# Performance work log

Hardware: AMD Instinct MI355X
Metric: run time of the kernel (lower is better)

Reference implementation:

```python
import jax, jax.numpy as jnp
import numpy as np

B, S, D, H = 512, 64, 1024, 16  # seq_len=64 fixed by Reshape([-1,8,8,d_model])
DH = D // H


def setup_inputs() -> dict:
    key = jax.random.key(0)
    ks = jax.random.split(key, 5)
    w_scale = 0.02  # keep pre-softmax logits / activations in a sane range
    return {
        "x": jax.random.normal(ks[0], (B, S, D), jnp.float32),
        "wq_w": jax.random.normal(ks[1], (D, D), jnp.float32) * w_scale,
        "wq_b": jnp.zeros((D,), jnp.float32),
        "wk_w": jax.random.normal(ks[2], (D, D), jnp.float32) * w_scale,
        "wk_b": jnp.zeros((D,), jnp.float32),
        "wv_w": jax.random.normal(ks[3], (D, D), jnp.float32) * w_scale,
        "wv_b": jnp.zeros((D,), jnp.float32),
        "wo_w": jax.random.normal(ks[4], (D, D), jnp.float32) * w_scale,
        "wo_b": jnp.zeros((D,), jnp.float32),
    }


def _split_heads(t):
    # [B, S, D] -> [B, H, S, DH]
    b, s, _ = t.shape
    return t.reshape(b, s, H, DH).transpose(0, 2, 1, 3)


def reference(x, wq_w, wq_b, wk_w, wk_b, wv_w, wv_b, wo_w, wo_b):
    b, s, d = x.shape
    q = _split_heads(x @ wq_w + wq_b)
    k = _split_heads(x @ wk_w + wk_b)
    v = _split_heads(x @ wv_w + wv_b)
    # NOTE: original scales by sqrt(d_model), not sqrt(depth)
    scores = jnp.einsum("bhqd,bhkd->bhqk", q, k) / jnp.sqrt(jnp.float32(d))
    # original 'padding mask': (scores == 0) * 1e-9 added to scores
    scores = scores + (scores == 0).astype(scores.dtype) * 1e-9
    attn = jax.nn.softmax(scores, axis=-1)
    ctx = jnp.einsum("bhqk,bhkd->bhqd", attn, v)  # [B, H, S, DH]
    ctx = ctx.transpose(0, 2, 1, 3).reshape(b, s, d)  # [B, S, D]
    # keras Dense(..., activation='gelu') uses exact (erf) gelu by default
    out = jax.nn.gelu(ctx @ wo_w + wo_b, approximate=False)
    # Reshape([-1, 8, 8, D]) then squeeze -> [B, 8, 8, D]
    return out.reshape(b, 8, 8, d)
```

## Files before the change

### kernel.cpp

```cpp
#include <hip/hip_runtime.h>
#include <cstdint>
#include <math.h>

typedef float f32x4 __attribute__((ext_vector_type(4)));
typedef __bf16 bf16x8 __attribute__((ext_vector_type(8)));
typedef unsigned short u16x8 __attribute__((ext_vector_type(8)));
typedef unsigned short u16x4 __attribute__((ext_vector_type(4)));

typedef __attribute__((address_space(1))) const void* gas_cvptr;
typedef __attribute__((address_space(3))) void* las_vptr;

#define WAITV8 asm volatile("s_waitcnt vmcnt(8)" ::: "memory")
#define WAITV4 asm volatile("s_waitcnt vmcnt(4)" ::: "memory")
#define WAITV0 asm volatile("s_waitcnt vmcnt(0)" ::: "memory")
#define WAITL0 asm volatile("s_waitcnt lgkmcnt(0)" ::: "memory")
#define WAITL4 asm volatile("s_waitcnt lgkmcnt(4)" ::: "memory")
#define SB()   __builtin_amdgcn_sched_barrier(0)
#define BAR()  __builtin_amdgcn_s_barrier()

__device__ __forceinline__ unsigned short f32_to_bf16(float f) {
  uint32_t u = __builtin_bit_cast(uint32_t, f);
  u += 0x7FFFu + ((u >> 16) & 1u);
  return (unsigned short)(u >> 16);
}

__device__ __forceinline__ bf16x8 ld_bf16x8(const unsigned short* p) {
  return __builtin_bit_cast(bf16x8, *(const u16x8*)p);
}

__global__ void cvt_x(const float* __restrict__ x, unsigned short* __restrict__ xb, int n4) {
  int stride = gridDim.x * blockDim.x;
  for (int i = blockIdx.x * blockDim.x + threadIdx.x; i < n4; i += stride) {
    float4 v = ((const float4*)x)[i];
    u16x4 o = { f32_to_bf16(v.x), f32_to_bf16(v.y), f32_to_bf16(v.z), f32_to_bf16(v.w) };
    ((u16x4*)xb)[i] = o;
  }
}

__global__ void cvt_w(const float* __restrict__ wq, const float* __restrict__ wk,
                      const float* __restrict__ wv, const float* __restrict__ wo,
                      unsigned short* __restrict__ wqkvT, unsigned short* __restrict__ woT) {
  const int z = blockIdx.z;
  const float* __restrict__ w = (z == 0) ? wq : (z == 1) ? wk : (z == 2) ? wv : wo;
  unsigned short* __restrict__ out = (z < 3) ? (wqkvT + (size_t)z * 1024 * 1024) : woT;
  __shared__ float tile[64][65];
  const int r0 = blockIdx.y * 64;
  const int c0 = blockIdx.x * 64;
  const int t = threadIdx.x;
#pragma unroll
  for (int i = 0; i < 4; i++) {
    int row = (t >> 4) + i * 16;
    int col = (t & 15) * 4;
    float4 v = *(const float4*)&w[(size_t)(r0 + row) * 1024 + c0 + col];
    tile[row][col] = v.x; tile[row][col + 1] = v.y;
    tile[row][col + 2] = v.z; tile[row][col + 3] = v.w;
  }
  __syncthreads();
#pragma unroll
  for (int i = 0; i < 2; i++) {
    int nr = (t >> 3) + i * 32;
    int kc = (t & 7) * 8;
    u16x8 o;
#pragma unroll
    for (int j = 0; j < 8; j++) o[j] = f32_to_bf16(tile[kc + j][nr]);
    *(u16x8*)&out[(size_t)(c0 + nr) * 1024 + r0 + kc] = o;
  }
}

template <int EPI>
__global__ __launch_bounds__(512, 2) void gemm256(
    const unsigned short* __restrict__ A, const unsigned short* __restrict__ Bt,
    const float* __restrict__ b0, const float* __restrict__ b1, const float* __restrict__ b2,
    unsigned short* __restrict__ Qb, unsigned short* __restrict__ Kb, unsigned short* __restrict__ Vb,
    float* __restrict__ Out, int Ncols, int K) {
  __shared__ __align__(16) unsigned short As[4][256][32];
  __shared__ __align__(16) unsigned short Bs[4][256][32];
  const int NT = K >> 5;
  const int nb = Ncols >> 8;
  const int nwg = gridDim.x;
  const int cpx = nwg >> 3;
  const int bid = blockIdx.x;
  const int wg = (bid & 7) * cpx + (bid >> 3);
  const int tm = wg / nb, tn = wg % nb;
  const int rowBase = tm << 8, colBase = tn << 8;
  const int t = threadIdx.x;
  const int lane = t & 63;
  const int w = t >> 6;
  const int li = lane & 15, lg = lane >> 4;
  const int wm = w >> 2, wn = w & 3;
  const int aRow0 = wm * 128;
  const int bRow0 = wn * 64;
  const int koff = ((lg ^ ((li >> 1) & 3)) << 3);

  const int c0 = t, c1 = t + 512;
  const int r0s = c0 >> 2, r1s = c1 >> 2;
  const int l0s = (c0 & 3) ^ ((r0s >> 1) & 3);
  const int l1s = (c1 & 3) ^ ((r1s >> 1) & 3);
  const unsigned short* gA0 = A + (size_t)(rowBase + r0s) * K + l0s * 8;
  const unsigned short* gA1 = A + (size_t)(rowBase + r1s) * K + l1s * 8;
  const unsigned short* gB0 = Bt + (size_t)(colBase + r0s) * K + l0s * 8;
  const unsigned short* gB1 = Bt + (size_t)(colBase + r1s) * K + l1s * 8;

#define STAGE_A(tile_) do { int b_ = (tile_) & 3; int kt_ = (tile_) << 5;                     \
    __builtin_amdgcn_global_load_lds((gas_cvptr)(gA0 + kt_),                                  \
        (las_vptr)(&As[b_][0][0] + c0 * 8), 16, 0, 0);                                        \
    __builtin_amdgcn_global_load_lds((gas_cvptr)(gA1 + kt_),                                  \
        (las_vptr)(&As[b_][0][0] + c1 * 8), 16, 0, 0); } while (0)
#define STAGE_B(tile_) do { int b_ = (tile_) & 3; int kt_ = (tile_) << 5;                     \
    __builtin_amdgcn_global_load_lds((gas_cvptr)(gB0 + kt_),                                  \
        (las_vptr)(&Bs[b_][0][0] + c0 * 8), 16, 0, 0);                                        \
    __builtin_amdgcn_global_load_lds((gas_cvptr)(gB1 + kt_),                                  \
        (las_vptr)(&Bs[b_][0][0] + c1 * 8), 16, 0, 0); } while (0)

  STAGE_A(0); STAGE_B(0);
  STAGE_A(1); STAGE_B(1);
  STAGE_A(2); STAGE_B(2);
  WAITV8;
  BAR();

  f32x4 acc[8][4] = {};

  for (int tt = 0; tt < NT; ++tt) {
    const unsigned short* ab = &As[tt & 3][0][0];
    const unsigned short* bb = &Bs[tt & 3][0][0];
    bf16x8 afA[4], bfrA[4], afB[4];
#pragma unroll
    for (int m = 0; m < 4; m++) afA[m] = ld_bf16x8(ab + (aRow0 + m * 16 + li) * 32 + koff);
#pragma unroll
    for (int n = 0; n < 4; n++) bfrA[n] = ld_bf16x8(bb + (bRow0 + n * 16 + li) * 32 + koff);
#pragma unroll
    for (int m = 0; m < 4; m++)
      afB[m] = ld_bf16x8(ab + (aRow0 + 64 + m * 16 + li) * 32 + koff);
    if (tt + 3 < NT) { STAGE_A(tt + 3); STAGE_B(tt + 3); }
    WAITL4;
    SB();
    __builtin_amdgcn_s_setprio(1);
#pragma unroll
    for (int m = 0; m < 4; m++)
#pragma unroll
      for (int n = 0; n < 4; n++)
        acc[m][n] = __builtin_amdgcn_mfma_f32_16x16x32_bf16(afA[m], bfrA[n], acc[m][n], 0, 0, 0);
    SB();
    WAITL0;
    SB();
#pragma unroll
    for (int m = 0; m < 4; m++)
#pragma unroll
      for (int n = 0; n < 4; n++)
        acc[4 + m][n] = __builtin_amdgcn_mfma_f32_16x16x32_bf16(afB[m], bfrA[n], acc[4 + m][n], 0, 0, 0);
    __builtin_amdgcn_s_setprio(0);
    if (tt <= NT - 4)      WAITV8;
    else if (tt == NT - 3) WAITV4;
    else                   WAITV0;
    BAR();
  }
#undef STAGE_A
#undef STAGE_B

  if (EPI == 0) {
    const int part = colBase >> 10;
    const float* __restrict__ bias = (part == 0) ? b0 : (part == 1) ? b1 : b2;
    unsigned short* __restrict__ dst = (part == 0) ? Qb : (part == 1) ? Kb : Vb;
#pragma unroll
    for (int mi = 0; mi < 8; mi++) {
      const int rowb = rowBase + aRow0 + mi * 16 + lg * 4;
#pragma unroll
      for (int r = 0; r < 4; r++) {
        const int row = rowb + r;
        const int b = row >> 6, s = row & 63;
#pragma unroll
        for (int n = 0; n < 4; n++) {
          const int col = colBase + bRow0 + n * 16 + li;
          const int within = col & 1023;
          const int h = within >> 6, dh = within & 63;
          float v = acc[mi][n][r] + bias[within];
          dst[(size_t)((b * 16 + h) * 64 + s) * 64 + dh] = f32_to_bf16(v);
        }
      }
    }
  } else {
#pragma unroll
    for (int mi = 0; mi < 8; mi++) {
      const int rowb = rowBase + aRow0 + mi * 16 + lg * 4;
#pragma unroll
      for (int r = 0; r < 4; r++) {
#pragma unroll
        for (int n = 0; n < 4; n++) {
          const int col = colBase + bRow0 + n * 16 + li;
          float v = acc[mi][n][r] + b0[col];
          v = 0.5f * v * (1.0f + erff(v * 0.70710678118654752f));
          Out[(size_t)(rowb + r) * 1024 + col] = v;
        }
      }
    }
  }
}

__global__ __launch_bounds__(256) void attn(
    const unsigned short* __restrict__ Qb, const unsigned short* __restrict__ Kb,
    const unsigned short* __restrict__ Vb, unsigned short* __restrict__ ctx) {
  __shared__ __align__(16) unsigned short Qs[64][72];
  __shared__ __align__(16) unsigned short Ks[64][72];
  __shared__ __align__(16) unsigned short Vt[64][72];
  __shared__ __align__(16) unsigned short Ps[64][72];
  const int bh = blockIdx.x;
  const int b = bh >> 4, h = bh & 15;
  const int t = threadIdx.x, lane = t & 63, w = t >> 6;
  const int li = lane & 15, lg = lane >> 4;
  const unsigned short* __restrict__ Qg = Qb + (size_t)bh * 4096;
  const unsigned short* __restrict__ Kg = Kb + (size_t)bh * 4096;
  const unsigned short* __restrict__ Vg = Vb + (size_t)bh * 4096;

#pragma unroll
  for (int i = 0; i < 2; i++) {
    const int c = t + i * 256;
    const int row = c >> 3, col8 = (c & 7) * 8;
    *(u16x8*)&Qs[row][col8] = *(const u16x8*)&Qg[row * 64 + col8];
    *(u16x8*)&Ks[row][col8] = *(const u16x8*)&Kg[row * 64 + col8];
    u16x8 v = *(const u16x8*)&Vg[row * 64 + col8];
#pragma unroll
    for (int j = 0; j < 8; j++) Vt[col8 + j][row] = v[j];
  }
  __syncthreads();

  f32x4 sc[4] = {};
#pragma unroll
  for (int ks = 0; ks < 2; ks++) {
    bf16x8 qa = ld_bf16x8(&Qs[w * 16 + li][ks * 32 + lg * 8]);
#pragma unroll
    for (int n = 0; n < 4; n++) {
      bf16x8 kf = ld_bf16x8(&Ks[n * 16 + li][ks * 32 + lg * 8]);
      sc[n] = __builtin_amdgcn_mfma_f32_16x16x32_bf16(qa, kf, sc[n], 0, 0, 0);
    }
  }

#pragma unroll
  for (int r = 0; r < 4; r++) {
    float v0 = sc[0][r] * 0.03125f, v1 = sc[1][r] * 0.03125f;
    float v2 = sc[2][r] * 0.03125f, v3 = sc[3][r] * 0.03125f;
    float mx = fmaxf(fmaxf(v0, v1), fmaxf(v2, v3));
#pragma unroll
    for (int off = 1; off < 16; off <<= 1) mx = fmaxf(mx, __shfl_xor(mx, off, 64));
    float e0 = __expf(v0 - mx), e1 = __expf(v1 - mx);
    float e2 = __expf(v2 - mx), e3 = __expf(v3 - mx);
    float sum = e0 + e1 + e2 + e3;
#pragma unroll
    for (int off = 1; off < 16; off <<= 1) sum += __shfl_xor(sum, off, 64);
    float is = 1.0f / sum;
    const int q = w * 16 + lg * 4 + r;
    Ps[q][0 * 16 + li] = f32_to_bf16(e0 * is);
    Ps[q][1 * 16 + li] = f32_to_bf16(e1 * is);
    Ps[q][2 * 16 + li] = f32_to_bf16(e2 * is);
    Ps[q][3 * 16 + li] = f32_to_bf16(e3 * is);
  }
  __syncthreads();

  f32x4 oc[4] = {};
#pragma unroll
  for (int ks = 0; ks < 2; ks++) {
    bf16x8 pa = ld_bf16x8(&Ps[w * 16 + li][ks * 32 + lg * 8]);
#pragma unroll
    for (int n = 0; n < 4; n++) {
      bf16x8 vf = ld_bf16x8(&Vt[n * 16 + li][ks * 32 + lg * 8]);
      oc[n] = __builtin_amdgcn_mfma_f32_16x16x32_bf16(pa, vf, oc[n], 0, 0, 0);
    }
  }
#pragma unroll
  for (int n = 0; n < 4; n++)
#pragma unroll
    for (int r = 0; r < 4; r++)
      ctx[(size_t)(b * 64 + w * 16 + lg * 4 + r) * 1024 + h * 64 + n * 16 + li] =
          f32_to_bf16(oc[n][r]);
}

extern "C" void kernel_launch(void* const* d_in, const int* in_sizes, int n_in,
                              void* d_out, int out_size, void* d_ws, size_t ws_size,
                              hipStream_t stream) {
  const float* x  = (const float*)d_in[0];
  const float* wq = (const float*)d_in[1];
  const float* bq = (const float*)d_in[2];
  const float* wk = (const float*)d_in[3];
  const float* bk = (const float*)d_in[4];
  const float* wv = (const float*)d_in[5];
  const float* bv = (const float*)d_in[6];
  const float* wo = (const float*)d_in[7];
  const float* bo = (const float*)d_in[8];
  float* out = (float*)d_out;

  const int D = 1024;
  const int M = in_sizes[0] / D;

  char* ws = (char*)d_ws;
  unsigned short* xb    = (unsigned short*)ws;
  unsigned short* wqkvT = (unsigned short*)(ws + (size_t)M * 1024 * 2);
  unsigned short* woT   = wqkvT + (size_t)3 * 1024 * 1024;
  unsigned short* Qb    = woT + (size_t)1024 * 1024;
  unsigned short* Kb    = Qb + (size_t)M * 1024;
  unsigned short* Vb    = Kb + (size_t)M * 1024;
  unsigned short* ctx   = xb;

  cvt_x<<<2048, 256, 0, stream>>>(x, xb, M * D / 4);
  cvt_w<<<dim3(16, 16, 4), 256, 0, stream>>>(wq, wk, wv, wo, wqkvT, woT);
  gemm256<0><<<(M / 256) * (3072 / 256), 512, 0, stream>>>(
      xb, wqkvT, bq, bk, bv, Qb, Kb, Vb, nullptr, 3072, 1024);
  attn<<<(M / 64) * 16, 256, 0, stream>>>(Qb, Kb, Vb, ctx);
  gemm256<1><<<(M / 256) * (1024 / 256), 512, 0, stream>>>(
      ctx, woT, bo, nullptr, nullptr, nullptr, nullptr, nullptr, out, 1024, 1024);
}
```

Before: 410.4 us.

## Deepen GEMM prefetch to four tiles and double-buffer LDS fragments in registers

The main GEMM loop now keeps four K-tiles of global-to-LDS loads in flight instead of three, using all four LDS buffers. It also adds two register fragment sets that alternate between tiles. The fragments for the next tile are read from LDS after the barrier, while the second half of the current tile's MFMAs run. The aim is to hide LDS read latency and global load latency behind matrix work. The cost is roughly double the fragment register usage under a 512-thread, 2-blocks-per-CU launch bound, and more complex wait-count logic.

```diff
diff --git a/kernel.cpp b/kernel.cpp
--- a/kernel.cpp
+++ b/kernel.cpp
@@ -10,11 +10,11 @@
 typedef __attribute__((address_space(1))) const void* gas_cvptr;
 typedef __attribute__((address_space(3))) void* las_vptr;
 
+#define WAITV12 asm volatile("s_waitcnt vmcnt(12)" ::: "memory")
 #define WAITV8 asm volatile("s_waitcnt vmcnt(8)" ::: "memory")
 #define WAITV4 asm volatile("s_waitcnt vmcnt(4)" ::: "memory")
 #define WAITV0 asm volatile("s_waitcnt vmcnt(0)" ::: "memory")
 #define WAITL0 asm volatile("s_waitcnt lgkmcnt(0)" ::: "memory")
-#define WAITL4 asm volatile("s_waitcnt lgkmcnt(4)" ::: "memory")
 #define SB()   __builtin_amdgcn_sched_barrier(0)
 #define BAR()  __builtin_amdgcn_s_barrier()
 
@@ -65,6 +65,20 @@
     for (int j = 0; j < 8; j++) o[j] = f32_to_bf16(tile[kc + j][nr]);
     *(u16x8*)&out[(size_t)(c0 + nr) * 1024 + r0 + kc] = o;
   }
+}
+
+struct Frags { bf16x8 afA[4], bfr[4], afB[4]; };
+
+__device__ __forceinline__ void read_frags(Frags& f, const unsigned short* ab,
+                                           const unsigned short* bb, int aRow0,
+                                           int bRow0, int li, int koff) {
+#pragma unroll
+  for (int m = 0; m < 4; m++) f.afA[m] = ld_bf16x8(ab + (aRow0 + m * 16 + li) * 32 + koff);
+#pragma unroll
+  for (int n = 0; n < 4; n++) f.bfr[n] = ld_bf16x8(bb + (bRow0 + n * 16 + li) * 32 + koff);
+#pragma unroll
+  for (int m = 0; m < 4; m++)
+    f.afB[m] = ld_bf16x8(ab + (aRow0 + 64 + m * 16 + li) * 32 + koff);
 }
 
 template <int EPI>
@@ -101,61 +115,58 @@
   const unsigned short* gB0 = Bt + (size_t)(colBase + r0s) * K + l0s * 8;
   const unsigned short* gB1 = Bt + (size_t)(colBase + r1s) * K + l1s * 8;
 
-#define STAGE_A(tile_) do { int b_ = (tile_) & 3; int kt_ = (tile_) << 5;                     \
+#define STAGE_AB(tile_) do { int b_ = (tile_) & 3; int kt_ = (tile_) << 5;                    \
     __builtin_amdgcn_global_load_lds((gas_cvptr)(gA0 + kt_),                                  \
         (las_vptr)(&As[b_][0][0] + c0 * 8), 16, 0, 0);                                        \
     __builtin_amdgcn_global_load_lds((gas_cvptr)(gA1 + kt_),                                  \
-        (las_vptr)(&As[b_][0][0] + c1 * 8), 16, 0, 0); } while (0)
-#define STAGE_B(tile_) do { int b_ = (tile_) & 3; int kt_ = (tile_) << 5;                     \
+        (las_vptr)(&As[b_][0][0] + c1 * 8), 16, 0, 0);                                        \
     __builtin_amdgcn_global_load_lds((gas_cvptr)(gB0 + kt_),                                  \
         (las_vptr)(&Bs[b_][0][0] + c0 * 8), 16, 0, 0);                                        \
     __builtin_amdgcn_global_load_lds((gas_cvptr)(gB1 + kt_),                                  \
         (las_vptr)(&Bs[b_][0][0] + c1 * 8), 16, 0, 0); } while (0)
 
-  STAGE_A(0); STAGE_B(0);
-  STAGE_A(1); STAGE_B(1);
-  STAGE_A(2); STAGE_B(2);
-  WAITV8;
+  STAGE_AB(0); STAGE_AB(1); STAGE_AB(2); STAGE_AB(3);
+  WAITV12;
   BAR();
 
   f32x4 acc[8][4] = {};
-
-  for (int tt = 0; tt < NT; ++tt) {
-    const unsigned short* ab = &As[tt & 3][0][0];
-    const unsigned short* bb = &Bs[tt & 3][0][0];
-    bf16x8 afA[4], bfrA[4], afB[4];
-#pragma unroll
-    for (int m = 0; m < 4; m++) afA[m] = ld_bf16x8(ab + (aRow0 + m * 16 + li) * 32 + koff);
-#pragma unroll
-    for (int n = 0; n < 4; n++) bfrA[n] = ld_bf16x8(bb + (bRow0 + n * 16 + li) * 32 + koff);
-#pragma unroll
-    for (int m = 0; m < 4; m++)
-      afB[m] = ld_bf16x8(ab + (aRow0 + 64 + m * 16 + li) * 32 + koff);
-    if (tt + 3 < NT) { STAGE_A(tt + 3); STAGE_B(tt + 3); }
-    WAITL4;
-    SB();
-    __builtin_amdgcn_s_setprio(1);
-#pragma unroll
-    for (int m = 0; m < 4; m++)
-#pragma unroll
-      for (int n = 0; n < 4; n++)
-        acc[m][n] = __builtin_amdgcn_mfma_f32_16x16x32_bf16(afA[m], bfrA[n], acc[m][n], 0, 0, 0);
-    SB();
-    WAITL0;
-    SB();
-#pragma unroll
-    for (int m = 0; m < 4; m++)
-#pragma unroll
-      for (int n = 0; n < 4; n++)
-        acc[4 + m][n] = __builtin_amdgcn_mfma_f32_16x16x32_bf16(afB[m], bfrA[n], acc[4 + m][n], 0, 0, 0);
-    __builtin_amdgcn_s_setprio(0);
-    if (tt <= NT - 4)      WAITV8;
-    else if (tt == NT - 3) WAITV4;
-    else                   WAITV0;
-    BAR();
-  }
-#undef STAGE_A
-#undef STAGE_B
+  Frags F0, F1;
+  read_frags(F0, &As[0][0][0], &Bs[0][0][0], aRow0, bRow0, li, koff);
+
+#define TILE_BODY(tt_, CUR, NXT) do {                                                         \
+    WAITL0; SB();                                                                             \
+    __builtin_amdgcn_s_setprio(1);                                                            \
+    _Pragma("unroll")                                                                         \
+    for (int m = 0; m < 4; m++)                                                               \
+      _Pragma("unroll")                                                                       \
+      for (int n = 0; n < 4; n++)                                                             \
+        acc[m][n] = __builtin_amdgcn_mfma_f32_16x16x32_bf16(CUR.afA[m], CUR.bfr[n],           \
+                                                            acc[m][n], 0, 0, 0);              \
+    __builtin_amdgcn_s_setprio(0);                                                            \
+    if ((tt_) <= NT - 4)      WAITV8;                                                         \
+    else if ((tt_) == NT - 3) WAITV4;                                                         \
+    else if ((tt_) == NT - 2) WAITV0;                                                         \
+    BAR();                                                                                    \
+    if ((tt_) + 1 < NT)                                                                       \
+      read_frags(NXT, &As[((tt_) + 1) & 3][0][0], &Bs[((tt_) + 1) & 3][0][0],                 \
+                 aRow0, bRow0, li, koff);                                                     \
+    if ((tt_) + 4 < NT) STAGE_AB((tt_) + 4);                                                  \
+    __builtin_amdgcn_s_setprio(1);                                                            \
+    _Pragma("unroll")                                                                         \
+    for (int m = 0; m < 4; m++)                                                               \
+      _Pragma("unroll")                                                                       \
+      for (int n = 0; n < 4; n++)                                                             \
+        acc[4 + m][n] = __builtin_amdgcn_mfma_f32_16x16x32_bf16(CUR.afB[m], CUR.bfr[n],       \
+                                                                acc[4 + m][n], 0, 0, 0);      \
+    __builtin_amdgcn_s_setprio(0);                                                            \
+  } while (0)
+
+  for (int tt = 0; tt < NT; tt += 2) {
+    TILE_BODY(tt, F0, F1);
+    TILE_BODY(tt + 1, F1, F0);
+  }
+#undef TILE_BODY
+#undef STAGE_AB
 
   if (EPI == 0) {
     const int part = colBase >> 10;
```

After: 409.8 us. No clear change (-0.2%).

## Shrink GEMM tile to 128x256 with 4 warps and 3-stage LDS pipeline

Applied to the files above, without the earlier changes.

The GEMM workgroup shrinks from a 256x256 tile with 8 waves to a 128x256 tile with 4 waves, each wave covering all 128 rows and 64 columns. The LDS ring drops from 4 stages to 3, and loads for the next tile are issued before the fragment reads, with the vmcnt waits adjusted to match. The aim is to double the number of workgroups and cut LDS use so more blocks fit per CU and the GPU is better filled. In exchange, each block reuses loaded data less and the prefetch depth is shallower.

```diff
diff --git a/kernel.cpp b/kernel.cpp
--- a/kernel.cpp
+++ b/kernel.cpp
@@ -10,11 +10,10 @@
 typedef __attribute__((address_space(1))) const void* gas_cvptr;
 typedef __attribute__((address_space(3))) void* las_vptr;
 
-#define WAITV8 asm volatile("s_waitcnt vmcnt(8)" ::: "memory")
-#define WAITV4 asm volatile("s_waitcnt vmcnt(4)" ::: "memory")
+#define WAITV6 asm volatile("s_waitcnt vmcnt(6)" ::: "memory")
 #define WAITV0 asm volatile("s_waitcnt vmcnt(0)" ::: "memory")
+#define WAITL4 asm volatile("s_waitcnt lgkmcnt(4)" ::: "memory")
 #define WAITL0 asm volatile("s_waitcnt lgkmcnt(0)" ::: "memory")
-#define WAITL4 asm volatile("s_waitcnt lgkmcnt(4)" ::: "memory")
 #define SB()   __builtin_amdgcn_sched_barrier(0)
 #define BAR()  __builtin_amdgcn_s_barrier()
 
@@ -68,13 +67,13 @@
 }
 
 template <int EPI>
-__global__ __launch_bounds__(512, 2) void gemm256(
+__global__ __launch_bounds__(256, 2) void gemm256(
     const unsigned short* __restrict__ A, const unsigned short* __restrict__ Bt,
     const float* __restrict__ b0, const float* __restrict__ b1, const float* __restrict__ b2,
     unsigned short* __restrict__ Qb, unsigned short* __restrict__ Kb, unsigned short* __restrict__ Vb,
     float* __restrict__ Out, int Ncols, int K) {
-  __shared__ __align__(16) unsigned short As[4][256][32];
-  __shared__ __align__(16) unsigned short Bs[4][256][32];
+  __shared__ __align__(16) unsigned short As[3][128][32];
+  __shared__ __align__(16) unsigned short Bs[3][256][32];
   const int NT = K >> 5;
   const int nb = Ncols >> 8;
   const int nwg = gridDim.x;
@@ -82,56 +81,57 @@
   const int bid = blockIdx.x;
   const int wg = (bid & 7) * cpx + (bid >> 3);
   const int tm = wg / nb, tn = wg % nb;
-  const int rowBase = tm << 8, colBase = tn << 8;
+  const int rowBase = tm << 7, colBase = tn << 8;
   const int t = threadIdx.x;
   const int lane = t & 63;
   const int w = t >> 6;
   const int li = lane & 15, lg = lane >> 4;
-  const int wm = w >> 2, wn = w & 3;
-  const int aRow0 = wm * 128;
-  const int bRow0 = wn * 64;
+  const int bRow0 = w << 6;
   const int koff = ((lg ^ ((li >> 1) & 3)) << 3);
 
-  const int c0 = t, c1 = t + 512;
-  const int r0s = c0 >> 2, r1s = c1 >> 2;
-  const int l0s = (c0 & 3) ^ ((r0s >> 1) & 3);
-  const int l1s = (c1 & 3) ^ ((r1s >> 1) & 3);
-  const unsigned short* gA0 = A + (size_t)(rowBase + r0s) * K + l0s * 8;
-  const unsigned short* gA1 = A + (size_t)(rowBase + r1s) * K + l1s * 8;
-  const unsigned short* gB0 = Bt + (size_t)(colBase + r0s) * K + l0s * 8;
-  const unsigned short* gB1 = Bt + (size_t)(colBase + r1s) * K + l1s * 8;
-
-#define STAGE_A(tile_) do { int b_ = (tile_) & 3; int kt_ = (tile_) << 5;                     \
+  const int cA0 = t, cA1 = t + 256;
+  const int cB0 = t, cB1 = t + 256, cB2 = t + 512, cB3 = t + 768;
+#define SRC(PTR, base_, c_) (PTR + (size_t)(base_ + ((c_) >> 2)) * K + \
+                             (((c_) & 3) ^ ((((c_) >> 2) >> 1) & 3)) * 8)
+  const unsigned short* gA0 = SRC(A, rowBase, cA0);
+  const unsigned short* gA1 = SRC(A, rowBase, cA1);
+  const unsigned short* gB0 = SRC(Bt, colBase, cB0);
+  const unsigned short* gB1 = SRC(Bt, colBase, cB1);
+  const unsigned short* gB2 = SRC(Bt, colBase, cB2);
+  const unsigned short* gB3 = SRC(Bt, colBase, cB3);
+#undef SRC
+
+#define STAGE_AB(tile_) do { int b_ = (tile_) % 3; int kt_ = (tile_) << 5;                    \
     __builtin_amdgcn_global_load_lds((gas_cvptr)(gA0 + kt_),                                  \
-        (las_vptr)(&As[b_][0][0] + c0 * 8), 16, 0, 0);                                        \
+        (las_vptr)(&As[b_][0][0] + cA0 * 8), 16, 0, 0);                                       \
     __builtin_amdgcn_global_load_lds((gas_cvptr)(gA1 + kt_),                                  \
-        (las_vptr)(&As[b_][0][0] + c1 * 8), 16, 0, 0); } while (0)
-#define STAGE_B(tile_) do { int b_ = (tile_) & 3; int kt_ = (tile_) << 5;                     \
+        (las_vptr)(&As[b_][0][0] + cA1 * 8), 16, 0, 0);                                       \
     __builtin_amdgcn_global_load_lds((gas_cvptr)(gB0 + kt_),                                  \
-        (las_vptr)(&Bs[b_][0][0] + c0 * 8), 16, 0, 0);                                        \
+        (las_vptr)(&Bs[b_][0][0] + cB0 * 8), 16, 0, 0);                                       \
     __builtin_amdgcn_global_load_lds((gas_cvptr)(gB1 + kt_),                                  \
-        (las_vptr)(&Bs[b_][0][0] + c1 * 8), 16, 0, 0); } while (0)
-
-  STAGE_A(0); STAGE_B(0);
-  STAGE_A(1); STAGE_B(1);
-  STAGE_A(2); STAGE_B(2);
-  WAITV8;
+        (las_vptr)(&Bs[b_][0][0] + cB1 * 8), 16, 0, 0);                                       \
+    __builtin_amdgcn_global_load_lds((gas_cvptr)(gB2 + kt_),                                  \
+        (las_vptr)(&Bs[b_][0][0] + cB2 * 8), 16, 0, 0);                                       \
+    __builtin_amdgcn_global_load_lds((gas_cvptr)(gB3 + kt_),                                  \
+        (las_vptr)(&Bs[b_][0][0] + cB3 * 8), 16, 0, 0); } while (0)
+
+  STAGE_AB(0); STAGE_AB(1);
+  WAITV6;
   BAR();
 
   f32x4 acc[8][4] = {};
 
   for (int tt = 0; tt < NT; ++tt) {
-    const unsigned short* ab = &As[tt & 3][0][0];
-    const unsigned short* bb = &Bs[tt & 3][0][0];
-    bf16x8 afA[4], bfrA[4], afB[4];
-#pragma unroll
-    for (int m = 0; m < 4; m++) afA[m] = ld_bf16x8(ab + (aRow0 + m * 16 + li) * 32 + koff);
-#pragma unroll
-    for (int n = 0; n < 4; n++) bfrA[n] = ld_bf16x8(bb + (bRow0 + n * 16 + li) * 32 + koff);
-#pragma unroll
-    for (int m = 0; m < 4; m++)
-      afB[m] = ld_bf16x8(ab + (aRow0 + 64 + m * 16 + li) * 32 + koff);
-    if (tt + 3 < NT) { STAGE_A(tt + 3); STAGE_B(tt + 3); }
+    if (tt + 2 < NT) STAGE_AB(tt + 2);
+    const unsigned short* ab = &As[tt % 3][0][0];
+    const unsigned short* bb = &Bs[tt % 3][0][0];
+    bf16x8 afA[4], bfr[4], afB[4];
+#pragma unroll
+    for (int m = 0; m < 4; m++) afA[m] = ld_bf16x8(ab + (m * 16 + li) * 32 + koff);
+#pragma unroll
+    for (int n = 0; n < 4; n++) bfr[n] = ld_bf16x8(bb + (bRow0 + n * 16 + li) * 32 + koff);
+#pragma unroll
+    for (int m = 0; m < 4; m++) afB[m] = ld_bf16x8(ab + (64 + m * 16 + li) * 32 + koff);
     WAITL4;
     SB();
     __builtin_amdgcn_s_setprio(1);
@@ -139,23 +139,22 @@
     for (int m = 0; m < 4; m++)
 #pragma unroll
       for (int n = 0; n < 4; n++)
-        acc[m][n] = __builtin_amdgcn_mfma_f32_16x16x32_bf16(afA[m], bfrA[n], acc[m][n], 0, 0, 0);
+        acc[m][n] = __builtin_amdgcn_mfma_f32_16x16x32_bf16(afA[m], bfr[n], acc[m][n], 0, 0, 0);
+    __builtin_amdgcn_s_setprio(0);
     SB();
     WAITL0;
     SB();
+    __builtin_amdgcn_s_setprio(1);
 #pragma unroll
     for (int m = 0; m < 4; m++)
 #pragma unroll
       for (int n = 0; n < 4; n++)
-        acc[4 + m][n] = __builtin_amdgcn_mfma_f32_16x16x32_bf16(afB[m], bfrA[n], acc[4 + m][n], 0, 0, 0);
+        acc[4 + m][n] = __builtin_amdgcn_mfma_f32_16x16x32_bf16(afB[m], bfr[n], acc[4 + m][n], 0, 0, 0);
     __builtin_amdgcn_s_setprio(0);
-    if (tt <= NT - 4)      WAITV8;
-    else if (tt == NT - 3) WAITV4;
-    else                   WAITV0;
+    if (tt < NT - 2) WAITV6; else WAITV0;
     BAR();
   }
-#undef STAGE_A
-#undef STAGE_B
+#undef STAGE_AB
 
   if (EPI == 0) {
     const int part = colBase >> 10;
@@ -163,7 +162,7 @@
     unsigned short* __restrict__ dst = (part == 0) ? Qb : (part == 1) ? Kb : Vb;
 #pragma unroll
     for (int mi = 0; mi < 8; mi++) {
-      const int rowb = rowBase + aRow0 + mi * 16 + lg * 4;
+      const int rowb = rowBase + mi * 16 + lg * 4;
 #pragma unroll
       for (int r = 0; r < 4; r++) {
         const int row = rowb + r;
@@ -181,7 +180,7 @@
   } else {
 #pragma unroll
     for (int mi = 0; mi < 8; mi++) {
-      const int rowb = rowBase + aRow0 + mi * 16 + lg * 4;
+      const int rowb = rowBase + mi * 16 + lg * 4;
 #pragma unroll
       for (int r = 0; r < 4; r++) {
 #pragma unroll
@@ -301,9 +300,9 @@
 
   cvt_x<<<2048, 256, 0, stream>>>(x, xb, M * D / 4);
   cvt_w<<<dim3(16, 16, 4), 256, 0, stream>>>(wq, wk, wv, wo, wqkvT, woT);
-  gemm256<0><<<(M / 256) * (3072 / 256), 512, 0, stream>>>(
+  gemm256<0><<<(M / 128) * (3072 / 256), 256, 0, stream>>>(
       xb, wqkvT, bq, bk, bv, Qb, Kb, Vb, nullptr, 3072, 1024);
   attn<<<(M / 64) * 16, 256, 0, stream>>>(Qb, Kb, Vb, ctx);
-  gemm256<1><<<(M / 256) * (1024 / 256), 512, 0, stream>>>(
+  gemm256<1><<<(M / 128) * (1024 / 256), 256, 0, stream>>>(
       ctx, woT, bo, nullptr, nullptr, nullptr, nullptr, nullptr, out, 1024, 1024);
 }
```

Measured after the change: 428.4 us. 1.04x slower.
